# Kernel optimization log

Hardware: AMD Instinct MI355X
Metric: run time of the kernel (lower is better)

## Reference

```python
import jax, jax.numpy as jnp
import numpy as np

EPS = 1e-08

def setup_inputs() -> dict:
    key = jax.random.key(0)
    k1, = jax.random.split(key, 1)
    B, C, H, W = 8, 128, 128, 256
    inp = jax.random.normal(k1, (B, C, H, W), dtype=jnp.float32)
    gain = jnp.ones((1, C, 1, 1), dtype=jnp.float32)
    bias = jnp.zeros((1, C, 1, 1), dtype=jnp.float32)
    return {"inp": inp, "gain": gain, "bias": bias}

def reference(inp, gain, bias):
    # LayerNorm over the last dim (W), then per-channel affine.
    # (Original torch code computes mean/var via a Python loop of adds;
    #  the intended math is a plain last-dim mean/variance.)
    mean = jnp.mean(inp, axis=-1, keepdims=True)
    centered = inp - mean
    var = jnp.mean(centered * centered, axis=-1, keepdims=True)
    std = jnp.sqrt(var + EPS)
    x = centered / std
    return x * gain + bias
```

## Files before the change

kernel.cpp:

```cpp
#include <hip/hip_runtime.h>
#include <hip/hip_bf16.h>


#define W_DIM 256
#define H_DIM 128
#define C_DIM 128
#define EPS 1e-8f

__global__ __launch_bounds__(256) void tLNv2_kernel(
    const float* __restrict__ inp,
    const float* __restrict__ gain,
    const float* __restrict__ bias,
    float* __restrict__ out)
{
    const int lane = threadIdx.x & 63;
    const int wave = threadIdx.x >> 6;
    const long long row = (long long)blockIdx.x * 4 + wave;

    const float4* __restrict__ in4 = (const float4*)(inp + row * W_DIM);
    float4 v = in4[lane];

    float s  = v.x + v.y + v.z + v.w;
    float sq = v.x * v.x + v.y * v.y + v.z * v.z + v.w * v.w;

    #pragma unroll
    for (int off = 1; off < 64; off <<= 1) {
        s  += __shfl_xor(s,  off, 64);
        sq += __shfl_xor(sq, off, 64);
    }

    const float mean = s * (1.0f / (float)W_DIM);
    const float var  = sq * (1.0f / (float)W_DIM) - mean * mean;
    const float rstd = rsqrtf(var + EPS);

    const int c = (int)((row >> 7) & (C_DIM - 1));
    const float g = gain[c];
    const float b = bias[c];

    float4 o;
    o.x = (v.x - mean) * rstd * g + b;
    o.y = (v.y - mean) * rstd * g + b;
    o.z = (v.z - mean) * rstd * g + b;
    o.w = (v.w - mean) * rstd * g + b;

    ((float4*)(out + row * W_DIM))[lane] = o;
}

extern "C" void kernel_launch(void* const* d_in, const int* in_sizes, int n_in,
                              void* d_out, int out_size, void* d_ws, size_t ws_size,
                              hipStream_t stream)
{
    const float* inp  = (const float*)d_in[0];
    const float* gain = (const float*)d_in[1];
    const float* bias = (const float*)d_in[2];
    float* out = (float*)d_out;

    const long long rows = (long long)in_sizes[0] / W_DIM;
    const int blocks = (int)(rows / 4);

    tLNv2_kernel<<<blocks, 256, 0, stream>>>(inp, gain, bias, out);
}
```

Measured before the change: 223.7 us.

## Map eight rows per wave with 8 float4 loads per lane

Each wave now handles eight rows: groups of eight lanes share a row, and each lane issues eight float4 loads. This cuts the cross-lane reduction from six shuffle stages to three and gives each thread more loads in flight. The affine step is folded into a single multiply-add by precomputing a scale and offset per row. The risks are higher register use, one eighth as many blocks, and each load instruction now touching eight rows at stride instead of one contiguous row.

Measured after the change: 233.0 us. 1.04x slower.

```diff
diff --git a/kernel.cpp b/kernel.cpp
--- a/kernel.cpp
+++ b/kernel.cpp
@@ -3,7 +3,6 @@
 
 
 #define W_DIM 256
-#define H_DIM 128
 #define C_DIM 128
 #define EPS 1e-8f
 
@@ -15,16 +14,26 @@
 {
     const int lane = threadIdx.x & 63;
     const int wave = threadIdx.x >> 6;
-    const long long row = (long long)blockIdx.x * 4 + wave;
+    const int l = lane & 7;
+    const int r = lane >> 3;
 
+    const long long row = (long long)blockIdx.x * 32 + wave * 8 + r;
     const float4* __restrict__ in4 = (const float4*)(inp + row * W_DIM);
-    float4 v = in4[lane];
 
-    float s  = v.x + v.y + v.z + v.w;
-    float sq = v.x * v.x + v.y * v.y + v.z * v.z + v.w * v.w;
+    float4 v[8];
+    #pragma unroll
+    for (int k = 0; k < 8; ++k)
+        v[k] = in4[k * 8 + l];
 
+    float s = 0.0f, sq = 0.0f;
     #pragma unroll
-    for (int off = 1; off < 64; off <<= 1) {
+    for (int k = 0; k < 8; ++k) {
+        s  += (v[k].x + v[k].y) + (v[k].z + v[k].w);
+        sq += (v[k].x * v[k].x + v[k].y * v[k].y)
+            + (v[k].z * v[k].z + v[k].w * v[k].w);
+    }
+    #pragma unroll
+    for (int off = 1; off < 8; off <<= 1) {
         s  += __shfl_xor(s,  off, 64);
         sq += __shfl_xor(sq, off, 64);
     }
@@ -34,16 +43,19 @@
     const float rstd = rsqrtf(var + EPS);
 
     const int c = (int)((row >> 7) & (C_DIM - 1));
-    const float g = gain[c];
-    const float b = bias[c];
+    const float g = gain[c] * rstd;
+    const float b = bias[c] - mean * g;
 
-    float4 o;
-    o.x = (v.x - mean) * rstd * g + b;
-    o.y = (v.y - mean) * rstd * g + b;
-    o.z = (v.z - mean) * rstd * g + b;
-    o.w = (v.w - mean) * rstd * g + b;
-
-    ((float4*)(out + row * W_DIM))[lane] = o;
+    float4* __restrict__ out4 = (float4*)(out + row * W_DIM);
+    #pragma unroll
+    for (int k = 0; k < 8; ++k) {
+        float4 o;
+        o.x = v[k].x * g + b;
+        o.y = v[k].y * g + b;
+        o.z = v[k].z * g + b;
+        o.w = v[k].w * g + b;
+        out4[k * 8 + l] = o;
+    }
 }
 
 extern "C" void kernel_launch(void* const* d_in, const int* in_sizes, int n_in,
@@ -56,7 +68,7 @@
     float* out = (float*)d_out;
 
     const long long rows = (long long)in_sizes[0] / W_DIM;
-    const int blocks = (int)(rows / 4);
+    const int blocks = (int)(rows / 32);
 
     tLNv2_kernel<<<blocks, 256, 0, stream>>>(inp, gain, bias, out);
 }
```
